# Kernel optimization log

Measured on AMD Instinct MI355X. Metric: run time of the kernel, lower is better.

The kernel has to match this reference:

```python
import jax, jax.numpy as jnp
import numpy as np

N = 20000      # nodes / tokens
H = 256        # hidden_size
NH = 8         # num_heads
HD = NH * H    # num_heads * hidden_size = 2048
EPS = 1e-5


def setup_inputs() -> dict:
    key = jax.random.key(0)
    ks = jax.random.split(key, 24)

    def lin_w(k, i, o):
        # xavier-ish scale for a Linear weight stored as [in, out]
        return jax.random.normal(k, (i, o), jnp.float32) * (1.0 / np.sqrt(i))

    inp = {
        'q': jax.random.normal(ks[0], (N, H), jnp.float32),
        'k': jax.random.normal(ks[1], (N, H), jnp.float32),
        'v': jax.random.normal(ks[2], (N, H), jnp.float32),
        'layer': 1,
        'Wq1': lin_w(ks[3], H, HD), 'bq1': jnp.zeros((HD,), jnp.float32),
        'Wk1': lin_w(ks[4], H, HD), 'bk1': jnp.zeros((HD,), jnp.float32),
        'Wq2': lin_w(ks[5], H, HD), 'bq2': jnp.zeros((HD,), jnp.float32),
        'Wk2': lin_w(ks[6], H, HD), 'bk2': jnp.zeros((HD,), jnp.float32),
        'Wv':  lin_w(ks[7], H, HD), 'bv':  jnp.zeros((HD,), jnp.float32),
        'ln_g': jnp.ones((HD,), jnp.float32),
        'ln_b': jnp.zeros((HD,), jnp.float32),
        'Wo': lin_w(ks[8], HD, H), 'bo': jnp.zeros((H,), jnp.float32),
        'lq1': jax.random.normal(ks[9], (H,), jnp.float32) * 0.1,
        'lk1': jax.random.normal(ks[10], (H,), jnp.float32) * 0.1,
        'lq2': jax.random.normal(ks[11], (H,), jnp.float32) * 0.1,
        'lk2': jax.random.normal(ks[12], (H,), jnp.float32) * 0.1,
    }
    return inp


def reference(q, k, v, layer, Wq1, bq1, Wk1, bk1, Wq2, bq2, Wk2, bk2,
              Wv, bv, ln_g, ln_b, Wo, bo, lq1, lk1, lq2, lk2):
    # projections: [N, H] -> [N, HD]
    q1 = q @ Wq1 + bq1
    k1 = k @ Wk1 + bk1
    q2 = q @ Wq2 + bq2
    k2 = k @ Wk2 + bk2
    vv = v @ Wv + bv

    # linear attention: K^T V -> [HD, HD]  (dropout is identity in eval mode)
    k1v = k1.T @ vv
    k2v = k2.T @ vv

    # lambda gating (scalars)
    lam1 = jnp.exp(jnp.sum(lq1 * lk1))
    lam2 = jnp.exp(jnp.sum(lq2 * lk2))
    lam_init = 0.8 - 0.6 * jnp.exp(jnp.asarray(-0.3 * layer, jnp.float32))
    lam_full = lam1 - lam2 + lam_init

    # Q @ (K^T V), differential subtraction: [N, HD]
    x = q1 @ k1v - lam_full * (q2 @ k2v)

    # LayerNorm over last dim (biased variance, eps=1e-5, like torch)
    mu = jnp.mean(x, axis=-1, keepdims=True)
    var = jnp.mean(jnp.square(x - mu), axis=-1, keepdims=True)
    x = (x - mu) / jnp.sqrt(var + EPS) * ln_g + ln_b

    x = x * (1.0 - lam_init)
    return x @ Wo + bo  # [N, H]
```

## Files before the change

### kernel.cpp

```cpp
#include <hip/hip_runtime.h>
#include <stdint.h>

typedef __bf16 bf16x8 __attribute__((ext_vector_type(8)));
typedef __bf16 bf16x4v __attribute__((ext_vector_type(4)));
typedef float f32x4 __attribute__((ext_vector_type(4)));
typedef float f32x2 __attribute__((ext_vector_type(2)));
typedef unsigned short u16x4 __attribute__((ext_vector_type(4)));
typedef unsigned short u16x8 __attribute__((ext_vector_type(8)));

#define NTOK 20000
#define NTP  20480
#define HIW  256
#define HD   2048
#define LDKP 66
#define LDS2 72

static __device__ __forceinline__ float bf2f(unsigned short h) {
  union { unsigned u; float f; } c; c.u = ((unsigned)h) << 16;
  return c.f;
}
static __device__ __forceinline__ unsigned short fbits(float x) {
  __bf16 h = (__bf16)x;
  return __builtin_bit_cast(unsigned short, h);
}

#define WRED(x) { x += __shfl_xor(x,32); x += __shfl_xor(x,16); x += __shfl_xor(x,8); \
                  x += __shfl_xor(x,4);  x += __shfl_xor(x,2);  x += __shfl_xor(x,1); }


__global__ __launch_bounds__(256) void k_front(
    const float* __restrict__ kk, const float* __restrict__ vv,
    const float* __restrict__ Wq1, const float* __restrict__ Wk1,
    const float* __restrict__ Wq2, const float* __restrict__ Wk2,
    const float* __restrict__ lq1, const float* __restrict__ lk1,
    const float* __restrict__ lq2, const float* __restrict__ lk2,
    const float* __restrict__ bq1, const float* __restrict__ bk1,
    const float* __restrict__ bq2, const float* __restrict__ bk2,
    const int* __restrict__ layer,
    unsigned short* __restrict__ kT, unsigned short* __restrict__ vT,
    float* __restrict__ skp, float* __restrict__ svp,
    unsigned short* __restrict__ Pc_part, float* __restrict__ scal,
    float* __restrict__ S) {
  __shared__ float SMEM[64][260];
  const int b = blockIdx.x, t = threadIdx.x;

  if (b < 640) {
    const int tile = b >> 1, m = b & 1;
    const float* src = m ? vv : kk;
    unsigned short* dstT = m ? vT : kT;
    float* sump = m ? svp : skp;
    #pragma unroll
    for (int i = 0; i < 16; ++i) {
      int ch = i * 256 + t;
      int row = ch >> 6, c4 = (ch & 63) * 4;
      int gtok = tile * 64 + row;
      f32x4 val = {0.f, 0.f, 0.f, 0.f};
      if (gtok < NTOK) val = *(const f32x4*)&src[(size_t)gtok * HIW + c4];
      *(f32x4*)&SMEM[row][c4] = val;
    }
    __syncthreads();
    float sum = 0.f;
    unsigned short cv[64];
    #pragma unroll
    for (int tok = 0; tok < 64; ++tok) {
      float x = SMEM[tok][t];
      sum += x;
      cv[tok] = fbits(x);
    }
    sump[tile * 256 + t] = sum;
    size_t base = (size_t)t * NTP + tile * 64;
    #pragma unroll
    for (int s = 0; s < 8; ++s)
      *(u16x8*)&dstT[base + s * 8] = *(const u16x8*)&cv[s * 8];
  } else if (b < 768) {
    unsigned short* Ak = (unsigned short*)SMEM;
    unsigned short* Bk = Ak + 128 * LDKP;
    const int idx = b - 640;
    const int pair = idx >> 6, rem = idx & 63;
    const int z = rem & 15, by = (rem >> 4) & 1, bx = (rem >> 5) & 1;
    const int i0 = bx * 128, j0 = by * 128;
    const int lane = t & 63, wave = t >> 6;
    const int wr = (wave >> 1) * 64, wc = (wave & 1) * 64;
    const int r15 = lane & 15, kg = (lane >> 4) * 8;
    const float* Wa = pair ? Wq2 : Wq1;
    const float* Wb = pair ? Wk2 : Wk1;
    f32x4 acc[4][4];
    #pragma unroll
    for (int m = 0; m < 4; ++m)
      #pragma unroll
      for (int n = 0; n < 4; ++n) acc[m][n] = (f32x4){0.f, 0.f, 0.f, 0.f};
    const int srow = t >> 1, sh = (t & 1) * 32;
    for (int kt = 0; kt < 2; ++kt) {
      const int kb = z * 128 + kt * 64 + sh;
      __syncthreads();
      #pragma unroll
      for (int c = 0; c < 8; ++c) {
        f32x4 a = *(const f32x4*)&Wa[(size_t)(i0 + srow) * HD + kb + c * 4];
        f32x4 bb = *(const f32x4*)&Wb[(size_t)(j0 + srow) * HD + kb + c * 4];
        bf16x4v oa, ob;
        #pragma unroll
        for (int u = 0; u < 4; ++u) { oa[u] = (__bf16)a[u]; ob[u] = (__bf16)bb[u]; }
        *(bf16x4v*)&Ak[srow * LDKP + sh + c * 4] = oa;
        *(bf16x4v*)&Bk[srow * LDKP + sh + c * 4] = ob;
      }
      __syncthreads();
      #pragma unroll
      for (int ks = 0; ks < 2; ++ks) {
        const int ko = ks * 32 + kg;
        bf16x8 ah[4], bh[4];
        #pragma unroll
        for (int m = 0; m < 4; ++m)
          ah[m] = *(const bf16x8*)&Ak[(wr + m * 16 + r15) * LDKP + ko];
        #pragma unroll
        for (int n = 0; n < 4; ++n)
          bh[n] = *(const bf16x8*)&Bk[(wc + n * 16 + r15) * LDKP + ko];
        #pragma unroll
        for (int m = 0; m < 4; ++m)
          #pragma unroll
          for (int n = 0; n < 4; ++n)
            acc[m][n] = __builtin_amdgcn_mfma_f32_16x16x32_bf16(ah[m], bh[n], acc[m][n], 0, 0, 0);
      }
    }
    const int rg = (lane >> 4) * 4;
    unsigned short* Pp = Pc_part + (size_t)(pair * 16 + z) * 65536;
    #pragma unroll
    for (int m = 0; m < 4; ++m)
      #pragma unroll
      for (int n = 0; n < 4; ++n)
        #pragma unroll
        for (int r = 0; r < 4; ++r)
          Pp[(i0 + wr + m * 16 + rg + r) * 256 + (j0 + wc + n * 16 + r15)] = fbits(acc[m][n][r]);
  } else if (b == 768) {
    float* red = (float*)SMEM;
    float p1 = lq1[t] * lk1[t], p2 = lq2[t] * lk2[t];
    float d1 = 0.f, d2 = 0.f;
    #pragma unroll
    for (int u = 0; u < 8; ++u) {
      d1 += bq1[t * 8 + u] * bk1[t * 8 + u];
      d2 += bq2[t * 8 + u] * bk2[t * 8 + u];
    }
    WRED(p1); WRED(p2); WRED(d1); WRED(d2);
    int w = t >> 6;
    if ((t & 63) == 0) { red[w] = p1; red[4 + w] = p2; red[8 + w] = d1; red[12 + w] = d2; }
    __syncthreads();
    if (t == 0) {
      float s1 = red[0] + red[1] + red[2] + red[3];
      float s2 = red[4] + red[5] + red[6] + red[7];
      float dd1 = red[8] + red[9] + red[10] + red[11];
      float dd2 = red[12] + red[13] + red[14] + red[15];
      float li = 0.8f - 0.6f * expf(-0.3f * (float)layer[0]);
      float lam = expf(s1) - expf(s2) + li;
      scal[0] = lam; scal[1] = -lam; scal[2] = 1.0f - li; scal[3] = li;
      scal[4] = dd1 - lam * dd2;
    }
  } else {
    const f32x4 z4 = {0.f, 0.f, 0.f, 0.f};
    #pragma unroll
    for (int i = 0; i < 64; ++i)
      *(f32x4*)&S[i * 1024 + t * 4] = z4;
  }
}

__global__ __launch_bounds__(512) void k_mid(
    const unsigned short* __restrict__ kT, const unsigned short* __restrict__ vT,
    float* __restrict__ S, const unsigned short* __restrict__ Pc_part,
    const float* __restrict__ skp, const float* __restrict__ svp,
    float* __restrict__ Pc, float* __restrict__ sk, float* __restrict__ sv,
    const float* __restrict__ Wk1, const float* __restrict__ Wk2,
    const float* __restrict__ Wq1, const float* __restrict__ Wq2,
    const float* __restrict__ bq1, const float* __restrict__ bq2,
    const float* __restrict__ bk1, const float* __restrict__ bk2,
    const float* __restrict__ scal, float* __restrict__ gc, float* __restrict__ uc) {
  __shared__ unsigned short SB[2 * 2 * 128 * LDS2];
  const int b = blockIdx.x, t = threadIdx.x;

  if (b < 256) {
    const int z = b & 63, by = (b >> 6) & 1, bx = (b >> 7) & 1;
    const int i0 = bx * 128, j0 = by * 128;
    const int tok0 = z * 320;
    const int lane = t & 63, wave = t >> 6;
    const int wr = (wave >> 1) * 32, wc = (wave & 1) * 64;
    const int r15 = lane & 15, kg = (lane >> 4) * 8;
    const int m = t >> 8;
    const int local = t & 255;
    const int row2 = local >> 1;
    const int koff = (local & 1) * 32;
    const unsigned short* srcT = m ? vT : kT;
    const size_t rbase = (size_t)((m ? j0 : i0) + row2) * NTP + tok0 + koff;
    const int lds_off = m * 128 * LDS2 + row2 * LDS2 + koff;

    f32x4 acc[2][4];
    #pragma unroll
    for (int mm = 0; mm < 2; ++mm)
      #pragma unroll
      for (int n = 0; n < 4; ++n) acc[mm][n] = (f32x4){0.f, 0.f, 0.f, 0.f};
    u16x8 rA[4], rB[4];

#define LOADT(R, KT)                                                          \
    { _Pragma("unroll")                                                       \
      for (int c = 0; c < 4; ++c)                                             \
        R[c] = *(const u16x8*)&srcT[rbase + (KT) * 64 + c * 8]; }
#define WRITET(BUF, R)                                                        \
    { unsigned short* d = &SB[(BUF) * 2 * 128 * LDS2 + lds_off];              \
      _Pragma("unroll")                                                       \
      for (int c = 0; c < 4; ++c) *(u16x8*)&d[c * 8] = R[c]; }

    LOADT(rA, 0)
    WRITET(0, rA)
    LOADT(rB, 1)
    asm volatile("s_waitcnt lgkmcnt(0)" ::: "memory");
    __builtin_amdgcn_s_barrier();

    #pragma unroll
    for (int kt = 0; kt < 5; ++kt) {
      const unsigned short* Ab = &SB[(kt & 1) * 2 * 128 * LDS2];
      const unsigned short* Bb = Ab + 128 * LDS2;
      __builtin_amdgcn_s_setprio(1);
      #pragma unroll
      for (int ks = 0; ks < 2; ++ks) {
        const int ko = ks * 32 + kg;
        bf16x8 ah[2], bh[4];
        #pragma unroll
        for (int mm = 0; mm < 2; ++mm)
          ah[mm] = *(const bf16x8*)&Ab[(wr + mm * 16 + r15) * LDS2 + ko];
        #pragma unroll
        for (int n = 0; n < 4; ++n)
          bh[n] = *(const bf16x8*)&Bb[(wc + n * 16 + r15) * LDS2 + ko];
        #pragma unroll
        for (int mm = 0; mm < 2; ++mm)
          #pragma unroll
          for (int n = 0; n < 4; ++n)
            acc[mm][n] = __builtin_amdgcn_mfma_f32_16x16x32_bf16(ah[mm], bh[n], acc[mm][n], 0, 0, 0);
      }
      __builtin_amdgcn_s_setprio(0);
      if (kt < 4) {
        if ((kt & 1) == 0) {
          WRITET(1, rB)
          if (kt + 2 <= 4) LOADT(rA, kt + 2)
        } else {
          WRITET(0, rA)
          if (kt + 2 <= 4) LOADT(rB, kt + 2)
        }
      }
      asm volatile("s_waitcnt lgkmcnt(0)" ::: "memory");
      __builtin_amdgcn_s_barrier();
    }
#undef LOADT
#undef WRITET
    const int rg = (lane >> 4) * 4;
    #pragma unroll
    for (int mm = 0; mm < 2; ++mm)
      #pragma unroll
      for (int n = 0; n < 4; ++n)
        #pragma unroll
        for (int r = 0; r < 4; ++r)
          atomicAdd(&S[(i0 + wr + mm * 16 + rg + r) * 256 + (j0 + wc + n * 16 + r15)],
                    acc[mm][n][r]);
  } else if (b < 288) {
    if (t < 256) {
      size_t idx = (size_t)(b - 256) * 2048 + t * 8;
      float s1[8] = {}, s2[8] = {};
      #pragma unroll 2
      for (int z = 0; z < 16; ++z) {
        u16x8 ha = *(const u16x8*)&Pc_part[(size_t)z * 65536 + idx];
        u16x8 hb = *(const u16x8*)&Pc_part[(size_t)(16 + z) * 65536 + idx];
        #pragma unroll
        for (int u = 0; u < 8; ++u) { s1[u] += bf2f(ha[u]); s2[u] += bf2f(hb[u]); }
      }
      float lam = scal[0];
      #pragma unroll
      for (int u = 0; u < 8; ++u) Pc[idx + u] = s1[u] - lam * s2[u];
    }
  } else if (b < 290) {
    if (t < 256) {
      const float* src = (b == 288) ? skp : svp;
      float s = 0.f;
      for (int z = 0; z < 320; ++z) s += src[z * 256 + t];
      if (b == 288) sk[t] = s; else sv[t] = s;
    }
  } else {
    if (t < 256) {
      int bb = b - 290, lane = t & 63, w = t >> 6;
      bool dogc = bb < 16;
      const float* A1 = dogc ? Wk1 : Wq1;
      const float* A2 = dogc ? Wk2 : Wq2;
      const float* x1 = dogc ? bq1 : bk1;
      const float* x2 = dogc ? bq2 : bk2;
      float* outv = dogc ? gc : uc;
      float lam = scal[0];
      int rb = (bb & 15) * 16 + w * 4;
      for (int q2 = 0; q2 < 4; ++q2) {
        int row = rb + q2;
        float s1 = 0.f, s2 = 0.f;
        #pragma unroll
        for (int c = 0; c < 8; ++c) {
          int kk2 = c * 256 + lane * 4;
          f32x4 a1 = *(const f32x4*)&A1[(size_t)row * HD + kk2];
          f32x4 a2 = *(const f32x4*)&A2[(size_t)row * HD + kk2];
          f32x4 v1 = *(const f32x4*)&x1[kk2];
          f32x4 v2 = *(const f32x4*)&x2[kk2];
          #pragma unroll
          for (int u = 0; u < 4; ++u) { s1 += a1[u] * v1[u]; s2 += a2[u] * v2[u]; }
        }
        WRED(s1); WRED(s2);
        if (lane == 0) outv[row] = s1 - lam * s2;
      }
    }
  }
}

__global__ __launch_bounds__(256) void k_ac(
    const float* __restrict__ Pc, const float* __restrict__ S,
    const float* __restrict__ gc, const float* __restrict__ sk,
    float* __restrict__ Ac, float* __restrict__ tc, float* __restrict__ rv,
    float* __restrict__ scal) {
  int b = blockIdx.x, t = threadIdx.x;
  if (b < 32) {
    __shared__ float Pt[32][68];
    __shared__ float St[64][68];
    int i0 = (b >> 2) * 32, j0 = (b & 3) * 64;
    int ti = t >> 5, tj = t & 31;
    float acc[4][2] = {};
    for (int kt = 0; kt < 256; kt += 64) {
      __syncthreads();
      {
        int rr = t >> 3, c8 = (t & 7) * 8;
        *(f32x4*)&Pt[rr][c8] = *(const f32x4*)&Pc[(i0 + rr) * 256 + kt + c8];
        *(f32x4*)&Pt[rr][c8 + 4] = *(const f32x4*)&Pc[(i0 + rr) * 256 + kt + c8 + 4];
      }
      {
        int rr = t >> 2, c16 = (t & 3) * 16;
        #pragma unroll
        for (int c = 0; c < 4; ++c)
          *(f32x4*)&St[rr][c16 + c * 4] = *(const f32x4*)&S[(kt + rr) * 256 + j0 + c16 + c * 4];
      }
      __syncthreads();
      #pragma unroll 8
      for (int k2 = 0; k2 < 64; ++k2) {
        float a[4];
        #pragma unroll
        for (int u = 0; u < 4; ++u) a[u] = Pt[ti * 4 + u][k2];
        f32x2 b2 = *(const f32x2*)&St[k2][tj * 2];
        #pragma unroll
        for (int u = 0; u < 4; ++u) { acc[u][0] += a[u] * b2[0]; acc[u][1] += a[u] * b2[1]; }
      }
    }
    #pragma unroll
    for (int u = 0; u < 4; ++u) {
      Ac[(i0 + ti * 4 + u) * 256 + j0 + tj * 2] = acc[u][0];
      Ac[(i0 + ti * 4 + u) * 256 + j0 + tj * 2 + 1] = acc[u][1];
    }
  } else if (b == 32) {
    int lane = t & 63, w = t >> 6;
    f32x4 sk4 = *(const f32x4*)&sk[lane * 4];
    for (int ii = 0; ii < 64; ++ii) {
      int i = w * 64 + ii;
      f32x4 p4 = *(const f32x4*)&Pc[i * 256 + lane * 4];
      float s = p4[0] * sk4[0] + p4[1] * sk4[1] + p4[2] * sk4[2] + p4[3] * sk4[3];
      WRED(s);
      if (lane == 0) tc[i] = s;
    }
  } else {
    float s0 = 0.f, s1 = 0.f, s2 = 0.f, s3 = 0.f;
    #pragma unroll 4
    for (int i = 0; i < 256; i += 4) {
      s0 += gc[i] * S[i * 256 + t];
      s1 += gc[i + 1] * S[(i + 1) * 256 + t];
      s2 += gc[i + 2] * S[(i + 2) * 256 + t];
      s3 += gc[i + 3] * S[(i + 3) * 256 + t];
    }
    rv[t] = (s0 + s1) + (s2 + s3);
    if (t < 64) {
      f32x4 g4 = *(const f32x4*)&gc[t * 4];
      f32x4 sk4 = *(const f32x4*)&sk[t * 4];
      float a = g4[0] * sk4[0] + g4[1] * sk4[1] + g4[2] * sk4[2] + g4[3] * sk4[3];
      WRED(a);
      if (t == 0) scal[5] = a;
    }
  }
}

__global__ __launch_bounds__(256) void k_gc(
    const float* __restrict__ Ac, const float* __restrict__ Wv,
    const float* __restrict__ tc, const float* __restrict__ uc,
    const float* __restrict__ sv, const float* __restrict__ rv,
    const float* __restrict__ bv, const float* __restrict__ scal,
    float* __restrict__ Gc, float* __restrict__ cc) {
  __shared__ float At[64][68];
  __shared__ float Bt[64][132];
  __shared__ float svr[256], rvr[256];
  int t = threadIdx.x;
  int i0 = blockIdx.x * 64, j0 = blockIdx.y * 128;
  int ti = t >> 5, tj = t & 31;
  svr[t] = sv[t]; rvr[t] = rv[t];
  float acc[8][4] = {};
  f32x4 swa = {0.f, 0.f, 0.f, 0.f}, sca = {0.f, 0.f, 0.f, 0.f};
  for (int kt = 0; kt < 256; kt += 64) {
    __syncthreads();
    {
      int rr = t >> 2, c16 = (t & 3) * 16;
      #pragma unroll
      for (int c = 0; c < 4; ++c)
        *(f32x4*)&At[rr][c16 + c * 4] = *(const f32x4*)&Ac[(i0 + rr) * 256 + kt + c16 + c * 4];
    }
    {
      int rr = t >> 2, c32 = (t & 3) * 32;
      #pragma unroll
      for (int c = 0; c < 8; ++c)
        *(f32x4*)&Bt[rr][c32 + c * 4] = *(const f32x4*)&Wv[(size_t)(kt + rr) * HD + j0 + c32 + c * 4];
    }
    __syncthreads();
    #pragma unroll 8
    for (int k2 = 0; k2 < 64; ++k2) {
      float a[8];
      #pragma unroll
      for (int u = 0; u < 8; ++u) a[u] = At[ti * 8 + u][k2];
      f32x4 b = *(const f32x4*)&Bt[k2][tj * 4];
      float svk = svr[kt + k2], rvk = rvr[kt + k2];
      swa += b * svk; sca += b * rvk;
      #pragma unroll
      for (int u = 0; u < 8; ++u)
        #pragma unroll
        for (int v = 0; v < 4; ++v) acc[u][v] += a[u] * b[v];
    }
  }
  int j = j0 + tj * 4;
  f32x4 bv4 = *(const f32x4*)&bv[j];
  f32x4 wnb;
  #pragma unroll
  for (int v = 0; v < 4; ++v) wnb[v] = swa[v] + 20000.0f * bv4[v];
  if (blockIdx.x == 0 && ti == 0) {
    float ac = scal[5], dc = scal[4];
    f32x4 ccv;
    #pragma unroll
    for (int v = 0; v < 4; ++v) ccv[v] = sca[v] + ac * bv4[v] + dc * wnb[v];
    *(f32x4*)&cc[j] = ccv;
  }
  #pragma unroll
  for (int u = 0; u < 8; ++u) {
    int i = i0 + ti * 8 + u;
    float tci = tc[i], uci = uc[i];
    f32x4 o;
    #pragma unroll
    for (int v = 0; v < 4; ++v)
      o[v] = acc[u][v] + tci * bv4[v] + uci * wnb[v];
    *(f32x4*)&Gc[(size_t)i * HD + j] = o;
  }
}

__global__ __launch_bounds__(256) void k_post(
    const float* __restrict__ Gc, const float* __restrict__ cc,
    const float* __restrict__ Wo, const float* __restrict__ g,
    const float* __restrict__ lnb, const float* __restrict__ scal_c,
    unsigned short* __restrict__ Bt2, float* __restrict__ M_part,
    float* __restrict__ Hc_part, float* __restrict__ scal) {
  __shared__ float SMEM[8768];
  int b = blockIdx.x, t = threadIdx.x;
  if (b < 17) {
    int lane = t & 63, w = t >> 6;
    if (b < 16) {
      int rb = b * 16 + w * 4;
      for (int q2 = 0; q2 < 4; ++q2) {
        int row = rb + q2;
        float s1 = 0.f, s2 = 0.f;
        #pragma unroll
        for (int c = 0; c < 8; ++c) {
          int kk2 = c * 256 + lane * 4;
          f32x4 g4 = *(const f32x4*)&Gc[(size_t)row * HD + kk2];
          f32x4 c4v = *(const f32x4*)&cc[kk2];
          #pragma unroll
          for (int u = 0; u < 4; ++u) { s1 += g4[u]; s2 += g4[u] * c4v[u]; }
        }
        WRED(s1); WRED(s2);
        if (lane == 0) {
          int base = ((256 + (row >> 5)) * 64 + ((row >> 3) & 3) * 16) * 8 + (row & 7);
          Bt2[base] = fbits(s1 * (1.0f / 2048.0f));
          Bt2[base + 8] = fbits(s2);
        }
      }
    } else {
      float s1 = 0.f, s2 = 0.f;
      #pragma unroll
      for (int c = 0; c < 2; ++c) {
        f32x4 v = *(const f32x4*)&cc[t * 8 + c * 4];
        #pragma unroll
        for (int u = 0; u < 4; ++u) { s1 += v[u]; s2 += v[u] * v[u]; }
      }
      WRED(s1); WRED(s2);
      if ((t & 63) == 0) { SMEM[t >> 6] = s1; SMEM[4 + (t >> 6)] = s2; }
      __syncthreads();
      if (t == 0) {
        scal[6] = SMEM[4] + SMEM[5] + SMEM[6] + SMEM[7];
        scal[7] = (SMEM[0] + SMEM[1] + SMEM[2] + SMEM[3]) * (1.0f / 2048.0f);
      }
      for (int idx = t; idx < 14 * 256; idx += 256) {
        int ci = idx >> 8, kk2 = idx & 255;
        int col = 514 + ci;
        Bt2[((256 + (kk2 >> 5)) * 64 + ((kk2 >> 3) & 3) * 16 + (col & 15)) * 8 + (kk2 & 7)] = 0;
      }
    }
  } else if (b < 81) {
    float (*Gi)[68] = (float(*)[68])SMEM;
    float (*Gj)[69] = (float(*)[69])(SMEM + 64 * 68);
    int idx = b - 17;
    int bx = idx & 3, by = (idx >> 2) & 3, z = idx >> 4;
    int i0 = bx * 64, j0 = by * 64;
    int ti = t >> 5, tj = t & 31;
    float acc[8][2] = {};
    for (int kt = 0; kt < 512; kt += 64) {
      int kb = z * 512 + kt;
      __syncthreads();
      {
        int rr = t >> 2, c16 = (t & 3) * 16;
        #pragma unroll
        for (int c = 0; c < 4; ++c) {
          *(f32x4*)&Gi[rr][c16 + c * 4] = *(const f32x4*)&Gc[(size_t)(i0 + rr) * HD + kb + c16 + c * 4];
          *(f32x4*)&Gj[rr][c16 + c * 4] = *(const f32x4*)&Gc[(size_t)(j0 + rr) * HD + kb + c16 + c * 4];
        }
      }
      __syncthreads();
      #pragma unroll 8
      for (int k2 = 0; k2 < 64; ++k2) {
        float a[8];
        #pragma unroll
        for (int u = 0; u < 8; ++u) a[u] = Gi[ti * 8 + u][k2];
        float b0 = Gj[tj * 2][k2], b1 = Gj[tj * 2 + 1][k2];
        #pragma unroll
        for (int u = 0; u < 8; ++u) { acc[u][0] += a[u] * b0; acc[u][1] += a[u] * b1; }
      }
    }
    #pragma unroll
    for (int u = 0; u < 8; ++u) {
      M_part[(size_t)z * 65536 + (i0 + ti * 8 + u) * 256 + j0 + tj * 2] = acc[u][0];
      M_part[(size_t)z * 65536 + (i0 + ti * 8 + u) * 256 + j0 + tj * 2 + 1] = acc[u][1];
    }
  } else {
    float (*At)[68] = (float(*)[68])SMEM;
    float (*Bt)[68] = (float(*)[68])(SMEM + 32 * 68);
    int idx = b - 81;
    int bx = idx % 9, rem = idx / 9, by = rem & 3, z = rem >> 2;
    int i0 = bx * 32, j0 = by * 64;
    float s2 = scal_c[2];
    int ti = t >> 5, tj = t & 31;
    float acc[4][2] = {};
    for (int kt = 0; kt < 512; kt += 64) {
      int kb = z * 512 + kt;
      __syncthreads();
      {
        int rr = t >> 3, c8 = (t & 7) * 8, gi = i0 + rr;
        #pragma unroll
        for (int h = 0; h < 8; h += 4) {
          f32x4 g4 = *(const f32x4*)&g[kb + c8 + h];
          f32x4 a;
          if (gi < 256) {
            f32x4 gg = *(const f32x4*)&Gc[(size_t)gi * HD + kb + c8 + h];
            #pragma unroll
            for (int u = 0; u < 4; ++u) a[u] = gg[u] * g4[u];
          } else if (gi == 256) {
            a = g4;
          } else if (gi == 257) {
            f32x4 c4v = *(const f32x4*)&cc[kb + c8 + h];
            #pragma unroll
            for (int u = 0; u < 4; ++u) a[u] = c4v[u] * g4[u];
          } else if (gi == 258) {
            a = *(const f32x4*)&lnb[kb + c8 + h];
          } else {
            a = (f32x4){0.f, 0.f, 0.f, 0.f};
          }
          *(f32x4*)&At[rr][c8 + h] = a;
        }
      }
      {
        int rr = t >> 2, c16 = (t & 3) * 16;
        #pragma unroll
        for (int c = 0; c < 4; ++c) {
          f32x4 bb = *(const f32x4*)&Wo[(size_t)(kb + rr) * 256 + j0 + c16 + c * 4];
          #pragma unroll
          for (int u = 0; u < 4; ++u) bb[u] *= s2;
          *(f32x4*)&Bt[rr][c16 + c * 4] = bb;
        }
      }
      __syncthreads();
      #pragma unroll 8
      for (int k2 = 0; k2 < 64; ++k2) {
        float a[4];
        #pragma unroll
        for (int u = 0; u < 4; ++u) a[u] = At[ti * 4 + u][k2];
        f32x2 b2 = *(const f32x2*)&Bt[k2][tj * 2];
        #pragma unroll
        for (int u = 0; u < 4; ++u) { acc[u][0] += a[u] * b2[0]; acc[u][1] += a[u] * b2[1]; }
      }
    }
    #pragma unroll
    for (int u = 0; u < 4; ++u) {
      Hc_part[(size_t)z * 73728 + (i0 + ti * 4 + u) * 256 + j0 + tj * 2] = acc[u][0];
      Hc_part[(size_t)z * 73728 + (i0 + ti * 4 + u) * 256 + j0 + tj * 2 + 1] = acc[u][1];
    }
  }
}

__global__ __launch_bounds__(256) void k_red2(
    const float* __restrict__ M_part, const float* __restrict__ Hc_part,
    const float* __restrict__ bo, unsigned short* __restrict__ Bt2,
    float* __restrict__ wbar, float* __restrict__ hcv, float* __restrict__ bcv) {
  int bi = blockIdx.x, z2 = blockIdx.y, t = threadIdx.x;
  if (z2 == 2) {
    if (bi != 0) return;
    float s0 = 0.f, s1 = 0.f, s2 = 0.f;
    #pragma unroll
    for (int z = 0; z < 4; ++z) {
      s0 += Hc_part[(size_t)z * 73728 + 256 * 256 + t];
      s1 += Hc_part[(size_t)z * 73728 + 257 * 256 + t];
      s2 += Hc_part[(size_t)z * 73728 + 258 * 256 + t];
    }
    wbar[t] = s0; hcv[t] = s1; bcv[t] = s2 + bo[t];
    return;
  }
  __shared__ unsigned short T[64][256];
  const float* src = z2 ? Hc_part : M_part;
  const size_t sp = z2 ? 73728 : 65536;
  const int base = z2 ? 256 : 0;
  for (int ii = 0; ii < 64; ++ii) {
    int i = bi * 64 + ii;
    float s = 0.f;
    #pragma unroll
    for (int z = 0; z < 4; ++z) s += src[z * sp + i * 256 + t];
    T[ii][t] = fbits(s);
  }
  __syncthreads();
  const int col = base + t;
  #pragma unroll
  for (int c = 0; c < 64; c += 8) {
    u16x8 o;
    #pragma unroll
    for (int u = 0; u < 8; ++u) o[u] = T[c + u][t];
    int kk0 = bi * 64 + c;
    int addr = (((col >> 4) * 8 + (kk0 >> 5)) * 64 + ((kk0 >> 3) & 3) * 16 + (col & 15)) * 8;
    *(u16x8*)&Bt2[addr] = o;
  }
}

__global__ __launch_bounds__(256) void k_out(
    const float* __restrict__ q, const unsigned short* __restrict__ Bt2,
    const float* __restrict__ hcv, const float* __restrict__ wbar,
    const float* __restrict__ bcv, const float* __restrict__ scal,
    float* __restrict__ out) {
  __shared__ unsigned short As[32 * 264];
  __shared__ float zbuf[32][260];
  __shared__ float sqp[2][32];
  __shared__ float muL[32], m2L[32];
  const int t = threadIdx.x, lane = t & 63, wave = t >> 6;
  const int row0 = blockIdx.x * 32;
  const int r15 = lane & 15, kg = lane >> 4;
  {
    int r = t >> 3;
    #pragma unroll
    for (int ci = 0; ci < 8; ++ci) {
      int col = ci * 32 + (t & 7) * 4;
      f32x4 v = *(const f32x4*)&q[(size_t)(row0 + r) * HIW + col];
      bf16x4v o;
      #pragma unroll
      for (int u = 0; u < 4; ++u) o[u] = (__bf16)v[u];
      *(bf16x4v*)&As[r * 264 + col] = o;
    }
  }
  __syncthreads();
  const int wc = wave * 128;
  const unsigned short* bbase = Bt2 + (size_t)(wave * 8) * 4096 + (size_t)lane * 8;
  f32x4 acc[2][9];
  #pragma unroll
  for (int m = 0; m < 2; ++m)
    #pragma unroll
    for (int n = 0; n < 9; ++n) acc[m][n] = (f32x4){0.f, 0.f, 0.f, 0.f};
  __builtin_amdgcn_s_setprio(1);
  #pragma unroll
  for (int ko = 0; ko < 8; ++ko) {
    bf16x8 af0 = *(const bf16x8*)&As[r15 * 264 + ko * 32 + kg * 8];
    bf16x8 af1 = *(const bf16x8*)&As[(16 + r15) * 264 + ko * 32 + kg * 8];
    #pragma unroll
    for (int ni = 0; ni < 9; ++ni) {
      if (ni == 8 && wave != 3) continue;
      bf16x8 bfr = *(const bf16x8*)&bbase[ni * 4096 + ko * 512];
      acc[0][ni] = __builtin_amdgcn_mfma_f32_16x16x32_bf16(af0, bfr, acc[0][ni], 0, 0, 0);
      acc[1][ni] = __builtin_amdgcn_mfma_f32_16x16x32_bf16(af1, bfr, acc[1][ni], 0, 0, 0);
    }
  }
  __builtin_amdgcn_s_setprio(0);
  if (wave < 2) {
    #pragma unroll
    for (int m = 0; m < 2; ++m)
      #pragma unroll
      for (int r = 0; r < 4; ++r) {
        int rowl = m * 16 + kg * 4 + r;
        float p = 0.f;
        #pragma unroll
        for (int ni = 0; ni < 8; ++ni) {
          int col = wc + ni * 16 + r15;
          p += acc[m][ni][r] * bf2f(As[rowl * 264 + col]);
        }
        p += __shfl_xor(p, 1); p += __shfl_xor(p, 2);
        p += __shfl_xor(p, 4); p += __shfl_xor(p, 8);
        if (r15 == 0) sqp[wave][rowl] = p;
      }
  } else {
    #pragma unroll
    for (int m = 0; m < 2; ++m)
      #pragma unroll
      for (int r = 0; r < 4; ++r) {
        int rowl = m * 16 + kg * 4 + r;
        #pragma unroll
        for (int ni = 0; ni < 8; ++ni)
          zbuf[rowl][(wc - 256) + ni * 16 + r15] = acc[m][ni][r];
      }
    if (wave == 3) {
      #pragma unroll
      for (int m = 0; m < 2; ++m)
        #pragma unroll
        for (int r = 0; r < 4; ++r) {
          int rowl = m * 16 + kg * 4 + r;
          if (r15 == 0) muL[rowl] = acc[m][8][r];
          if (r15 == 1) m2L[rowl] = acc[m][8][r];
        }
    }
  }
  __syncthreads();
  const float css = scal[6], cbar = scal[7];
  #pragma unroll
  for (int i = 0; i < 8; ++i) {
    const int row = i * 4 + wave;
    const int c4 = lane * 4;
    float mu = muL[row] + cbar;
    float ss = sqp[0][row] + sqp[1][row] + 2.0f * m2L[row] + css;
    float var = ss * (1.0f / 2048.0f) - mu * mu;
    float rstd = rsqrtf(var + 1e-5f);
    f32x4 zv = *(const f32x4*)&zbuf[row][c4];
    f32x4 h4 = *(const f32x4*)&hcv[c4];
    f32x4 w4 = *(const f32x4*)&wbar[c4];
    f32x4 b4 = *(const f32x4*)&bcv[c4];
    f32x4 o;
    #pragma unroll
    for (int u = 0; u < 4; ++u)
      o[u] = rstd * (zv[u] + h4[u] - mu * w4[u]) + b4[u];
    *(f32x4*)&out[(size_t)(row0 + row) * HIW + c4] = o;
  }
}

extern "C" void kernel_launch(void* const* d_in, const int* in_sizes, int n_in,
                              void* d_out, int out_size, void* d_ws, size_t ws_size,
                              hipStream_t stream) {
  const float* q   = (const float*)d_in[0];
  const float* k   = (const float*)d_in[1];
  const float* v   = (const float*)d_in[2];
  const int* layer = (const int*)d_in[3];
  const float* Wq1 = (const float*)d_in[4];  const float* bq1 = (const float*)d_in[5];
  const float* Wk1 = (const float*)d_in[6];  const float* bk1 = (const float*)d_in[7];
  const float* Wq2 = (const float*)d_in[8];  const float* bq2 = (const float*)d_in[9];
  const float* Wk2 = (const float*)d_in[10]; const float* bk2 = (const float*)d_in[11];
  const float* Wv  = (const float*)d_in[12]; const float* bv  = (const float*)d_in[13];
  const float* lng = (const float*)d_in[14]; const float* lnb = (const float*)d_in[15];
  const float* Wo  = (const float*)d_in[16]; const float* bo  = (const float*)d_in[17];
  const float* lq1 = (const float*)d_in[18]; const float* lk1 = (const float*)d_in[19];
  const float* lq2 = (const float*)d_in[20]; const float* lk2 = (const float*)d_in[21];

  char* p = (char*)d_ws;
  unsigned short* kT = (unsigned short*)p;
  float* M_part  = (float*)p;
  float* Hc_part = (float*)(p + 1048576);
  unsigned short* Bt2 = (unsigned short*)(p + 1048576 + 1179648);
  p += (size_t)256 * NTP * 2;
  unsigned short* vT = (unsigned short*)p;
  float* Gc = (float*)p;
  p += (size_t)256 * NTP * 2;
  float* skp = (float*)p;     p += (size_t)320 * 256 * 4;
  float* svp = (float*)p;     p += (size_t)320 * 256 * 4;
  unsigned short* Pc_part = (unsigned short*)p; p += (size_t)32 * 65536 * 2;
  float* S  = (float*)p;      p += 65536 * 4;
  float* Pc = (float*)p;      p += 65536 * 4;
  float* sk = (float*)p;      p += 1024;
  float* sv = (float*)p;      p += 1024;
  float* gc = (float*)p;      p += 1024;
  float* uc = (float*)p;      p += 1024;
  float* tc = (float*)p;      p += 1024;
  float* rv = (float*)p;      p += 1024;
  float* cc = (float*)p;      p += 2048 * 4;
  float* Ac = (float*)p;      p += 65536 * 4;
  float* wbar = (float*)p;    p += 1024;
  float* hcv  = (float*)p;    p += 1024;
  float* bcv  = (float*)p;    p += 1024;
  float* scal = (float*)p;    p += 256;

  const dim3 b256(256);
  k_front<<<dim3(770), b256, 0, stream>>>(k, v, Wq1, Wk1, Wq2, Wk2,
      lq1, lk1, lq2, lk2, bq1, bk1, bq2, bk2, layer, kT, vT, skp, svp, Pc_part, scal, S);
  k_mid<<<dim3(322), dim3(512), 0, stream>>>(kT, vT, S, Pc_part, skp, svp, Pc, sk, sv,
      Wk1, Wk2, Wq1, Wq2, bq1, bq2, bk1, bk2, scal, gc, uc);
  k_ac<<<dim3(34), b256, 0, stream>>>(Pc, S, gc, sk, Ac, tc, rv, scal);
  k_gc<<<dim3(4, 16), b256, 0, stream>>>(Ac, Wv, tc, uc, sv, rv, bv, scal, Gc, cc);
  k_post<<<dim3(225), b256, 0, stream>>>(Gc, cc, Wo, lng, lnb, scal, Bt2, M_part, Hc_part, scal);
  k_red2<<<dim3(4, 3), b256, 0, stream>>>(M_part, Hc_part, bo, Bt2, wbar, hcv, bcv);
  k_out<<<dim3(625), b256, 0, stream>>>(q, Bt2, hcv, wbar, bcv, scal, (float*)d_out);
}
```

Before: 180.6 us.

## Tile-major transposed K/V layout and split k_out across eight waves

The transposed bf16 K and V buffers are stored tile-major, so each 64-token tile is one contiguous 32 KB block rather than rows strided by NTP. The k_mid loads then read contiguous chunks per tile, which should improve DRAM locality. k_out goes from 256 to 512 threads: each wave now handles 64 output columns instead of 128, which halves accumulator registers and doubles the number of waves issuing MFMAs. The sum-of-squares partials grow to four slots. The cost is more LDS and barrier pressure per block.

```diff
diff --git a/kernel.cpp b/kernel.cpp
--- a/kernel.cpp
+++ b/kernel.cpp
@@ -14,6 +14,7 @@
 #define HD   2048
 #define LDKP 66
 #define LDS2 72
+#define TSZ  16384
 
 static __device__ __forceinline__ float bf2f(unsigned short h) {
   union { unsigned u; float f; } c; c.u = ((unsigned)h) << 16;
@@ -68,7 +69,7 @@
       cv[tok] = fbits(x);
     }
     sump[tile * 256 + t] = sum;
-    size_t base = (size_t)t * NTP + tile * 64;
+    size_t base = (size_t)tile * TSZ + (size_t)t * 64;
     #pragma unroll
     for (int s = 0; s < 8; ++s)
       *(u16x8*)&dstT[base + s * 8] = *(const u16x8*)&cv[s * 8];
@@ -177,7 +178,6 @@
   if (b < 256) {
     const int z = b & 63, by = (b >> 6) & 1, bx = (b >> 7) & 1;
     const int i0 = bx * 128, j0 = by * 128;
-    const int tok0 = z * 320;
     const int lane = t & 63, wave = t >> 6;
     const int wr = (wave >> 1) * 32, wc = (wave & 1) * 64;
     const int r15 = lane & 15, kg = (lane >> 4) * 8;
@@ -186,7 +186,7 @@
     const int row2 = local >> 1;
     const int koff = (local & 1) * 32;
     const unsigned short* srcT = m ? vT : kT;
-    const size_t rbase = (size_t)((m ? j0 : i0) + row2) * NTP + tok0 + koff;
+    const size_t tbase = (size_t)(5 * z) * TSZ + (size_t)((m ? j0 : i0) + row2) * 64 + koff;
     const int lds_off = m * 128 * LDS2 + row2 * LDS2 + koff;
 
     f32x4 acc[2][4];
@@ -199,7 +199,7 @@
 #define LOADT(R, KT)                                                          \
     { _Pragma("unroll")                                                       \
       for (int c = 0; c < 4; ++c)                                             \
-        R[c] = *(const u16x8*)&srcT[rbase + (KT) * 64 + c * 8]; }
+        R[c] = *(const u16x8*)&srcT[tbase + (size_t)(KT) * TSZ + c * 8]; }
 #define WRITET(BUF, R)                                                        \
     { unsigned short* d = &SB[(BUF) * 2 * 128 * LDS2 + lds_off];              \
       _Pragma("unroll")                                                       \
@@ -640,53 +640,55 @@
   }
 }
 
-__global__ __launch_bounds__(256) void k_out(
+__global__ __launch_bounds__(512) void k_out(
     const float* __restrict__ q, const unsigned short* __restrict__ Bt2,
     const float* __restrict__ hcv, const float* __restrict__ wbar,
     const float* __restrict__ bcv, const float* __restrict__ scal,
     float* __restrict__ out) {
   __shared__ unsigned short As[32 * 264];
   __shared__ float zbuf[32][260];
-  __shared__ float sqp[2][32];
+  __shared__ float sqp[4][32];
   __shared__ float muL[32], m2L[32];
   const int t = threadIdx.x, lane = t & 63, wave = t >> 6;
   const int row0 = blockIdx.x * 32;
   const int r15 = lane & 15, kg = lane >> 4;
   {
-    int r = t >> 3;
-    #pragma unroll
-    for (int ci = 0; ci < 8; ++ci) {
-      int col = ci * 32 + (t & 7) * 4;
-      f32x4 v = *(const f32x4*)&q[(size_t)(row0 + r) * HIW + col];
+    #pragma unroll
+    for (int i = 0; i < 4; ++i) {
+      int ch = i * 512 + t;
+      int row = ch >> 6, c4 = (ch & 63) * 4;
+      f32x4 v = *(const f32x4*)&q[(size_t)(row0 + row) * HIW + c4];
       bf16x4v o;
       #pragma unroll
       for (int u = 0; u < 4; ++u) o[u] = (__bf16)v[u];
-      *(bf16x4v*)&As[r * 264 + col] = o;
+      *(bf16x4v*)&As[row * 264 + c4] = o;
     }
   }
   __syncthreads();
-  const int wc = wave * 128;
-  const unsigned short* bbase = Bt2 + (size_t)(wave * 8) * 4096 + (size_t)lane * 8;
-  f32x4 acc[2][9];
+  const bool isM = wave < 4;
+  const int wcol = isM ? wave * 64 : 256 + (wave - 4) * 64;
+  const int grp0 = wcol >> 4;
+  f32x4 acc[2][5];
   #pragma unroll
   for (int m = 0; m < 2; ++m)
     #pragma unroll
-    for (int n = 0; n < 9; ++n) acc[m][n] = (f32x4){0.f, 0.f, 0.f, 0.f};
+    for (int n = 0; n < 5; ++n) acc[m][n] = (f32x4){0.f, 0.f, 0.f, 0.f};
   __builtin_amdgcn_s_setprio(1);
   #pragma unroll
   for (int ko = 0; ko < 8; ++ko) {
     bf16x8 af0 = *(const bf16x8*)&As[r15 * 264 + ko * 32 + kg * 8];
     bf16x8 af1 = *(const bf16x8*)&As[(16 + r15) * 264 + ko * 32 + kg * 8];
     #pragma unroll
-    for (int ni = 0; ni < 9; ++ni) {
-      if (ni == 8 && wave != 3) continue;
-      bf16x8 bfr = *(const bf16x8*)&bbase[ni * 4096 + ko * 512];
+    for (int ni = 0; ni < 5; ++ni) {
+      if (ni == 4 && wave != 7) continue;
+      const int grp = (ni == 4) ? 32 : grp0 + ni;
+      bf16x8 bfr = *(const bf16x8*)&Bt2[(size_t)(grp * 8 + ko) * 512 + lane * 8];
       acc[0][ni] = __builtin_amdgcn_mfma_f32_16x16x32_bf16(af0, bfr, acc[0][ni], 0, 0, 0);
       acc[1][ni] = __builtin_amdgcn_mfma_f32_16x16x32_bf16(af1, bfr, acc[1][ni], 0, 0, 0);
     }
   }
   __builtin_amdgcn_s_setprio(0);
-  if (wave < 2) {
+  if (isM) {
     #pragma unroll
     for (int m = 0; m < 2; ++m)
       #pragma unroll
@@ -694,8 +696,8 @@
         int rowl = m * 16 + kg * 4 + r;
         float p = 0.f;
         #pragma unroll
-        for (int ni = 0; ni < 8; ++ni) {
-          int col = wc + ni * 16 + r15;
+        for (int ni = 0; ni < 4; ++ni) {
+          int col = wcol + ni * 16 + r15;
           p += acc[m][ni][r] * bf2f(As[rowl * 264 + col]);
         }
         p += __shfl_xor(p, 1); p += __shfl_xor(p, 2);
@@ -709,28 +711,29 @@
       for (int r = 0; r < 4; ++r) {
         int rowl = m * 16 + kg * 4 + r;
         #pragma unroll
-        for (int ni = 0; ni < 8; ++ni)
-          zbuf[rowl][(wc - 256) + ni * 16 + r15] = acc[m][ni][r];
-      }
-    if (wave == 3) {
+        for (int ni = 0; ni < 4; ++ni)
+          zbuf[rowl][(wcol - 256) + ni * 16 + r15] = acc[m][ni][r];
+      }
+    if (wave == 7) {
       #pragma unroll
       for (int m = 0; m < 2; ++m)
         #pragma unroll
         for (int r = 0; r < 4; ++r) {
           int rowl = m * 16 + kg * 4 + r;
-          if (r15 == 0) muL[rowl] = acc[m][8][r];
-          if (r15 == 1) m2L[rowl] = acc[m][8][r];
+          if (r15 == 0) muL[rowl] = acc[m][4][r];
+          if (r15 == 1) m2L[rowl] = acc[m][4][r];
         }
     }
   }
   __syncthreads();
   const float css = scal[6], cbar = scal[7];
   #pragma unroll
-  for (int i = 0; i < 8; ++i) {
-    const int row = i * 4 + wave;
+  for (int i = 0; i < 4; ++i) {
+    const int row = i * 8 + wave;
     const int c4 = lane * 4;
     float mu = muL[row] + cbar;
-    float ss = sqp[0][row] + sqp[1][row] + 2.0f * m2L[row] + css;
+    float ss = (sqp[0][row] + sqp[1][row]) + (sqp[2][row] + sqp[3][row]) +
+               2.0f * m2L[row] + css;
     float var = ss * (1.0f / 2048.0f) - mu * mu;
     float rstd = rsqrtf(var + 1e-5f);
     f32x4 zv = *(const f32x4*)&zbuf[row][c4];
@@ -798,5 +801,5 @@
   k_gc<<<dim3(4, 16), b256, 0, stream>>>(Ac, Wv, tc, uc, sv, rv, bv, scal, Gc, cc);
   k_post<<<dim3(225), b256, 0, stream>>>(Gc, cc, Wo, lng, lnb, scal, Bt2, M_part, Hc_part, scal);
   k_red2<<<dim3(4, 3), b256, 0, stream>>>(M_part, Hc_part, bo, Bt2, wbar, hcv, bcv);
-  k_out<<<dim3(625), b256, 0, stream>>>(q, Bt2, hcv, wbar, bcv, scal, (float*)d_out);
-}
+  k_out<<<dim3(625), dim3(512), 0, stream>>>(q, Bt2, hcv, wbar, bcv, scal, (float*)d_out);
+}
```

New measurement: 172.7 us. 1.05x faster.
